# Kernel optimization log

Hardware: AMD Instinct MI355X
Metric: run time of the kernel (lower is better)

The kernel has to match this reference:

```python
import jax, jax.numpy as jnp
import numpy as np
import math

B, T, H, NH, BLOCK = 2, 2048, 1024, 16, 2048
HS = H // NH  # 64, even as required by RoPE


def make_rope_cache(hs, block):
    # positions t = 1..block (note: source starts at 1, not 0)
    t = np.arange(1, block + 1, dtype=np.float32)[:, None]          # (block, 1)
    i = np.arange(1, hs // 2 + 1, dtype=np.float32)[None, :]        # (1, hs/2)
    theta = (1.0 / 10000.0) ** (2.0 * (i - 1.0) / hs)               # (1, hs/2)
    ang = t * theta                                                  # (block, hs/2)
    return jnp.asarray(np.stack([np.cos(ang), np.sin(ang)], axis=-1))  # (block, hs/2, 2)


def setup_inputs() -> dict:
    key = jax.random.key(0)
    ks = jax.random.split(key, 10)
    s = 0.02
    x = jax.random.normal(ks[0], (B, T, H), jnp.float32)
    masks = jax.random.randint(ks[1], (B, T), 0, 2, jnp.int32)  # 1 = padding token
    Wq = jax.random.normal(ks[2], (H, H), jnp.float32) * s
    bq = jnp.zeros((H,), jnp.float32)
    Wk = jax.random.normal(ks[3], (H, H), jnp.float32) * s
    bk = jnp.zeros((H,), jnp.float32)
    Wv = jax.random.normal(ks[4], (H, H), jnp.float32) * s
    bv = jnp.zeros((H,), jnp.float32)
    Wo = jax.random.normal(ks[5], (H, H), jnp.float32) * s  # final_proj, no bias
    rope = make_rope_cache(HS, BLOCK)
    return {"x": x, "masks": masks, "Wq": Wq, "bq": bq, "Wk": Wk, "bk": bk,
            "Wv": Wv, "bv": bv, "Wo": Wo, "rope": rope}


def _apply_rope(x, cos, sin):
    # x: (B, nh, T, hs); cos/sin: (T, hs/2) broadcast over (B, nh)
    xe, xo = x[..., ::2], x[..., 1::2]
    real = cos * xe - sin * xo
    imag = sin * xe + cos * xo
    return jnp.stack([real, imag], axis=-1).reshape(x.shape)


def reference(x, masks, Wq, bq, Wk, bk, Wv, bv, Wo, rope):
    Bn, Tn, Hn = x.shape
    nh, hs = NH, Hn // NH

    def proj(W, b):
        # torch Linear: x @ W.T + b -> (B, nh, T, hs)
        return (x @ W.T + b).reshape(Bn, Tn, nh, hs).transpose(0, 2, 1, 3)

    Q, K, V = proj(Wq, bq), proj(Wk, bk), proj(Wv, bv)
    cos, sin = rope[:Tn, :, 0], rope[:Tn, :, 1]
    Q = _apply_rope(Q, cos, sin)
    K = _apply_rope(K, cos, sin)

    att = jnp.einsum('bhqd,bhkd->bhqk', Q, K) * (1.0 / math.sqrt(hs))
    causal = jnp.tril(jnp.ones((Tn, Tn), bool))
    att = jnp.where(causal[None, None, :, :], att, -1e10)          # causal mask
    att = jnp.where((masks == 1)[:, None, None, :], -1e10, att)   # padding mask on keys
    att = jax.nn.softmax(att, axis=-1)

    y = jnp.einsum('bhqk,bhkd->bhqd', att, V)
    y = y.transpose(0, 2, 1, 3).reshape(Bn, Tn, Hn)
    return y @ Wo.T  # final_proj has no bias
```

## Files before the change

kernel.cpp:

```cpp
#include <hip/hip_runtime.h>

typedef short short8 __attribute__((ext_vector_type(8)));
typedef float floatx4 __attribute__((ext_vector_type(4)));
typedef unsigned short u16;
typedef unsigned long long u64;

#define Tn 2048
#define Kdim 1024
#define QSCALE 0.18033688011112042f
#define FIXEDMAX 20.0f

__device__ inline u16 f2bf(float x) {
    union { float f; unsigned u; } c; c.f = x;
    unsigned u = c.u;
    u += 0x7fffu + ((u >> 16) & 1u);
    return (u16)(u >> 16);
}
__device__ inline float bf2f(u16 h) {
    union { unsigned u; float f; } c; c.u = ((unsigned)h) << 16;
    return c.f;
}
__device__ inline floatx4 mfma16(short8 a, short8 b, floatx4 c) {
    return __builtin_amdgcn_mfma_f32_16x16x32_bf16(a, b, c, 0, 0, 0);
}
__device__ inline void async16(const void* g, void* l) {
    __builtin_amdgcn_global_load_lds((const __attribute__((address_space(1))) void*)g,
                                     (__attribute__((address_space(3))) void*)l, 16, 0, 0);
}

__global__ __launch_bounds__(256) void cvt_all_k(
    const float* __restrict__ x, const float* __restrict__ wq, const float* __restrict__ wk,
    const float* __restrict__ wv, const float* __restrict__ wo, u16* __restrict__ dst)
{
    int i = blockIdx.x * 256 + threadIdx.x;
    const float* s; int off;
    if (i < 1048576) { s = x; off = i; }
    else {
        int j = i - 1048576; int seg = j >> 18; off = j & 262143;
        s = (seg == 0) ? wq : (seg == 1) ? wk : (seg == 2) ? wv : wo;
    }
    float4 v = ((const float4*)s)[off];
    u64 pk = (u64)f2bf(v.x) | ((u64)f2bf(v.y) << 16) | ((u64)f2bf(v.z) << 32) | ((u64)f2bf(v.w) << 48);
    ((u64*)dst)[i] = pk;
}

__global__ __launch_bounds__(256, 5) void gemm_qkv_k(
    const u16* __restrict__ A,
    const u16* __restrict__ W0, const u16* __restrict__ W1, const u16* __restrict__ W2,
    const float* __restrict__ b0, const float* __restrict__ b1, const float* __restrict__ b2,
    u16* o0, u16* o1, u16* o2,
    const float2* __restrict__ rope)
{
    int z = blockIdx.z;
    const u16* W = (z == 0) ? W0 : (z == 1 ? W1 : W2);
    const float* bias = (z == 0) ? b0 : (z == 1 ? b1 : b2);
    u16* outp = (z == 0) ? o0 : (z == 1 ? o1 : o2);

    __shared__ __align__(16) char lds[24576];
    int tid = threadIdx.x;
    int w = tid >> 6, lane = tid & 63, quad = lane >> 4, l15 = lane & 15;
    int m0 = blockIdx.y * 128, n0 = blockIdx.x * 64;
    int wm = w * 32;

    floatx4 acc[2][4];
    floatx4 vzero = {0.f, 0.f, 0.f, 0.f};
#pragma unroll
    for (int i = 0; i < 2; ++i)
#pragma unroll
        for (int j = 0; j < 4; ++j) acc[i][j] = vzero;

    for (int k0 = 0; k0 < Kdim; k0 += 64) {
#pragma unroll
        for (int j = 0; j < 4; ++j) {
            int f = j * 256 + tid, r = f >> 3, c = (f & 7) ^ (r & 7);
            async16(A + (size_t)(m0 + r) * Kdim + k0 + c * 8, lds + j * 4096 + w * 1024);
        }
#pragma unroll
        for (int j = 0; j < 2; ++j) {
            int f = j * 256 + tid, r = f >> 3, c = (f & 7) ^ (r & 7);
            async16(W + (size_t)(n0 + r) * Kdim + k0 + c * 8, lds + 16384 + j * 4096 + w * 1024);
        }
        __syncthreads();
        short8 af[2][2];
#pragma unroll
        for (int mt = 0; mt < 2; ++mt) {
            int ra = wm + mt * 16 + l15;
            const char* pa = lds + ra * 128;
#pragma unroll
            for (int ks = 0; ks < 2; ++ks)
                af[mt][ks] = *(const short8*)(pa + (((ks * 4 + quad) ^ (ra & 7)) << 4));
        }
#pragma unroll
        for (int ks = 0; ks < 2; ++ks)
#pragma unroll
            for (int nt = 0; nt < 4; ++nt) {
                int rb = nt * 16 + l15;
                short8 bf = *(const short8*)(lds + 16384 + rb * 128 + (((ks * 4 + quad) ^ (rb & 7)) << 4));
                acc[0][nt] = mfma16(af[0][ks], bf, acc[0][nt]);
                acc[1][nt] = mfma16(af[1][ks], bf, acc[1][nt]);
            }
        __syncthreads();
    }

    int mbase = m0 + wm;
    if (z <= 1) {
        float osc = (z == 0) ? QSCALE : 1.0f;
#pragma unroll
        for (int nt = 0; nt < 4; ++nt) {
            int col = n0 + nt * 16 + l15;
            float bv = bias[col];
            int p = (col & 63) >> 1;
#pragma unroll
            for (int mt = 0; mt < 2; ++mt) {
                floatx4 a = acc[mt][nt];
#pragma unroll
                for (int r = 0; r < 4; ++r) {
                    int row = mbase + mt * 16 + quad * 4 + r;
                    float v = a[r] + bv;
                    float ov = __shfl_xor(v, 1, 64);
                    float2 cs = rope[(row & (Tn - 1)) * 32 + p];
                    float res = (cs.x * v + ((lane & 1) ? cs.y * ov : -cs.y * ov)) * osc;
                    float pres = __shfl_xor(res, 1, 64);
                    if (!(lane & 1)) {
                        unsigned pk = (unsigned)f2bf(res) | ((unsigned)f2bf(pres) << 16);
                        *(unsigned*)(outp + (size_t)row * 1024 + col) = pk;
                    }
                }
            }
        }
    } else {
#pragma unroll
        for (int nt = 0; nt < 4; ++nt) {
            int col = n0 + nt * 16 + l15;
            float bv = bias[col];
#pragma unroll
            for (int mt = 0; mt < 2; ++mt) {
                floatx4 a = acc[mt][nt];
                int row0 = mbase + mt * 16 + quad * 4;
                int bb = row0 >> 11, t0 = row0 & (Tn - 1);
                u64 pk = (u64)f2bf(a[0] + bv) | ((u64)f2bf(a[1] + bv) << 16)
                       | ((u64)f2bf(a[2] + bv) << 32) | ((u64)f2bf(a[3] + bv) << 48);
                *(u64*)(outp + (size_t)(bb * 1024 + col) * Tn + t0) = pk;
            }
        }
    }
}

__global__ __launch_bounds__(256, 4) void gemm_o_k(
    const u16* __restrict__ A, const u16* __restrict__ W, float* __restrict__ out)
{
    __shared__ __align__(16) char lds[16384];
    int tid = threadIdx.x;
    int w = tid >> 6, lane = tid & 63, quad = lane >> 4, l15 = lane & 15;
    int m0 = blockIdx.y * 64, n0 = blockIdx.x * 64;
    int wm = (w >> 1) * 32, wn = (w & 1) * 32;

    floatx4 acc[2][2];
    floatx4 vzero = {0.f, 0.f, 0.f, 0.f};
#pragma unroll
    for (int i = 0; i < 2; ++i)
#pragma unroll
        for (int j = 0; j < 2; ++j) acc[i][j] = vzero;

    for (int k0 = 0; k0 < Kdim; k0 += 64) {
#pragma unroll
        for (int j = 0; j < 2; ++j) {
            int f = j * 256 + tid, r = f >> 3, c = (f & 7) ^ (r & 7);
            async16(A + (size_t)(m0 + r) * Kdim + k0 + c * 8, lds + j * 4096 + w * 1024);
            async16(W + (size_t)(n0 + r) * Kdim + k0 + c * 8, lds + 8192 + j * 4096 + w * 1024);
        }
        __syncthreads();
        short8 af[2][2];
#pragma unroll
        for (int mt = 0; mt < 2; ++mt) {
            int ra = wm + mt * 16 + l15;
            const char* pa = lds + ra * 128;
#pragma unroll
            for (int ks = 0; ks < 2; ++ks)
                af[mt][ks] = *(const short8*)(pa + (((ks * 4 + quad) ^ (ra & 7)) << 4));
        }
#pragma unroll
        for (int ks = 0; ks < 2; ++ks)
#pragma unroll
            for (int nt = 0; nt < 2; ++nt) {
                int rb = wn + nt * 16 + l15;
                short8 bf = *(const short8*)(lds + 8192 + rb * 128 + (((ks * 4 + quad) ^ (rb & 7)) << 4));
                acc[0][nt] = mfma16(af[0][ks], bf, acc[0][nt]);
                acc[1][nt] = mfma16(af[1][ks], bf, acc[1][nt]);
            }
        __syncthreads();
    }

#pragma unroll
    for (int nt = 0; nt < 2; ++nt) {
        int col = n0 + wn + nt * 16 + l15;
#pragma unroll
        for (int mt = 0; mt < 2; ++mt) {
            floatx4 a = acc[mt][nt];
#pragma unroll
            for (int r = 0; r < 4; ++r) {
                int row = m0 + wm + mt * 16 + quad * 4 + r;
                out[(size_t)row * 1024 + col] = a[r];
            }
        }
    }
}

__global__ __launch_bounds__(64) void vmean_k(const u16* __restrict__ Vt, float* __restrict__ vmean) {
    int row = blockIdx.x;
    int lane = threadIdx.x;
    const u16* p = Vt + (size_t)row * Tn;
    float s = 0.f;
    for (int i = lane * 8; i < Tn; i += 512) {
        short8 v = *(const short8*)(p + i);
#pragma unroll
        for (int j = 0; j < 8; ++j) s += bf2f((u16)v[j]);
    }
#pragma unroll
    for (int off = 1; off < 64; off <<= 1) s += __shfl_xor(s, off, 64);
    if (lane == 0) vmean[row] = s * (1.f / 2048.f);
}

__global__ __launch_bounds__(256) void flash_k(
    const u16* __restrict__ Qb, const u16* __restrict__ Kb, const u16* __restrict__ Vt,
    const int* __restrict__ masks, const float* __restrict__ vmean, u16* __restrict__ Yb)
{
    int bid = blockIdx.x;
    int bh = (bid & 7) * 4 + ((bid >> 3) & 3);
    int qt = 31 - (bid >> 5);
    int b = bh >> 4, h = bh & 15;
    int tid = threadIdx.x, w = tid >> 6, lane = tid & 63, quad = lane >> 4, l15 = lane & 15;
    int sc = (lane & 7) ^ (lane >> 3);

    __shared__ __align__(16) u16 ldsK[2][64 * 64];
    __shared__ __align__(16) u16 ldsV[2][64 * 64];
    __shared__ __align__(16) u16 ldsP[4][16 * 64];

    int ktiles = qt + 1;
    unsigned blo = 0, bhi = 0;
    for (int j = 0; j < ktiles; ++j) {
        u64 mk = __ballot(masks[b * Tn + j * 64 + lane] != 0);
        if (lane == j) { blo = (unsigned)mk; bhi = (unsigned)(mk >> 32); }
    }

    auto stage = [&](int bb, int k0) {
#pragma unroll
        for (int j = 0; j < 2; ++j) {
            int row = j * 32 + w * 8 + (lane >> 3);
            const u16* gk = Kb + (size_t)(b * Tn + k0 + row) * 1024 + h * 64 + sc * 8;
            async16(gk, (char*)&ldsK[bb][0] + (j * 32 + w * 8) * 128);
            const u16* gv = Vt + (size_t)(b * 1024 + h * 64 + row) * Tn + k0 + sc * 8;
            async16(gv, (char*)&ldsV[bb][0] + (j * 32 + w * 8) * 128);
        }
    };
    floatx4 vzero = {0.f, 0.f, 0.f, 0.f};

    int q0 = qt * 64 + w * 16;
    short8 qf[2];
    {
        const u16* qp = Qb + (size_t)(b * Tn + q0 + l15) * 1024 + h * 64 + quad * 8;
        qf[0] = *(const short8*)qp;
        qf[1] = *(const short8*)(qp + 32);
    }
    floatx4 o[4];
    float lsum[4] = {0.f, 0.f, 0.f, 0.f};
#pragma unroll
    for (int i = 0; i < 4; ++i) o[i] = vzero;

    stage(0, 0);
    for (int kt = 0; kt < ktiles; ++kt) {
        int k0 = kt * 64;
        int bb = kt & 1;
        __syncthreads();

        short8 kf[4][2], vf[4][2];
#pragma unroll
        for (int f = 0; f < 4; ++f) {
            int key = f * 16 + l15;
            const char* kbase = (const char*)&ldsK[bb][0] + key * 128;
            const char* vbase = (const char*)&ldsV[bb][0] + key * 128;
#pragma unroll
            for (int ks = 0; ks < 2; ++ks) {
                int slot = ((quad + ks * 4) ^ (key & 7)) << 4;
                kf[f][ks] = *(const short8*)(kbase + slot);
                vf[f][ks] = *(const short8*)(vbase + slot);
            }
        }
        if (kt + 1 < ktiles) stage(bb ^ 1, k0 + 64);

        floatx4 s[4];
#pragma unroll
        for (int f = 0; f < 4; ++f) {
            s[f] = mfma16(qf[0], kf[f][0], vzero);
            s[f] = mfma16(qf[1], kf[f][1], s[f]);
        }

        unsigned mlo = __shfl(blo, kt, 64), mhi = __shfl(bhi, kt, 64);
        int mb[4];
        mb[0] = (mlo >> l15) & 1; mb[1] = (mlo >> (l15 + 16)) & 1;
        mb[2] = (mhi >> l15) & 1; mb[3] = (mhi >> (l15 + 16)) & 1;

        if (k0 + 63 <= q0) {
#pragma unroll
            for (int r = 0; r < 4; ++r) {
                float psum = 0.f;
#pragma unroll
                for (int f = 0; f < 4; ++f) {
                    float v = mb[f] ? -1e10f : s[f][r];
                    float p = __builtin_amdgcn_exp2f(v - FIXEDMAX);
                    psum += p;
                    unsigned u = __float_as_uint(p) + 0x8000u;
                    int row = quad * 4 + r, key = f * 16 + l15;
                    ldsP[w][0] = ldsP[w][0];
                    *((u16*)((char*)&ldsP[w][0] + row * 128 +
                             ((((key >> 3) ^ (row & 7))) << 4) + (key & 7) * 2)) = (u16)(u >> 16);
                }
                lsum[r] += psum;
            }
        } else {
#pragma unroll
            for (int r = 0; r < 4; ++r) {
                int lim = q0 + quad * 4 + r - k0;
                float psum = 0.f;
#pragma unroll
                for (int f = 0; f < 4; ++f) {
                    float v = (16 * f + l15 > lim || mb[f]) ? -1e10f : s[f][r];
                    float p = __builtin_amdgcn_exp2f(v - FIXEDMAX);
                    psum += p;
                    unsigned u = __float_as_uint(p) + 0x8000u;
                    int row = quad * 4 + r, key = f * 16 + l15;
                    *((u16*)((char*)&ldsP[w][0] + row * 128 +
                             ((((key >> 3) ^ (row & 7))) << 4) + (key & 7) * 2)) = (u16)(u >> 16);
                }
                lsum[r] += psum;
            }
        }
        __asm__ volatile("s_waitcnt lgkmcnt(0)" ::: "memory");
        short8 pf0 = *(const short8*)((const char*)&ldsP[w][0] + l15 * 128 + ((quad ^ (l15 & 7)) << 4));
        short8 pf1 = *(const short8*)((const char*)&ldsP[w][0] + l15 * 128 + (((quad + 4) ^ (l15 & 7)) << 4));
#pragma unroll
        for (int nb = 0; nb < 4; ++nb) {
            o[nb] = mfma16(pf0, vf[nb][0], o[nb]);
            o[nb] = mfma16(pf1, vf[nb][1], o[nb]);
        }
    }

#pragma unroll
    for (int r = 0; r < 4; ++r) {
        int qq = q0 + quad * 4 + r;
        float l = lsum[r];
#pragma unroll
        for (int off = 1; off < 16; off <<= 1) l += __shfl_xor(l, off, 64);
        bool degen = (l == 0.f);
        float linv = 1.0f / l;
#pragma unroll
        for (int nb = 0; nb < 4; ++nb) {
            int d = nb * 16 + l15;
            float val = degen ? vmean[b * 1024 + h * 64 + d] : o[nb][r] * linv;
            float pv = __shfl_xor(val, 1, 64);
            if (!(lane & 1)) {
                unsigned pk = (unsigned)f2bf(val) | ((unsigned)f2bf(pv) << 16);
                *(unsigned*)(Yb + (size_t)(b * Tn + qq) * 1024 + h * 64 + d) = pk;
            }
        }
    }
}

extern "C" void kernel_launch(void* const* d_in, const int* in_sizes, int n_in,
                              void* d_out, int out_size, void* d_ws, size_t ws_size,
                              hipStream_t stream) {
    const float* x  = (const float*)d_in[0];
    const int* masks = (const int*)d_in[1];
    const float* Wq = (const float*)d_in[2];
    const float* bq = (const float*)d_in[3];
    const float* Wk = (const float*)d_in[4];
    const float* bk = (const float*)d_in[5];
    const float* Wv = (const float*)d_in[6];
    const float* bv = (const float*)d_in[7];
    const float* Wo = (const float*)d_in[8];
    const float2* rope = (const float2*)d_in[9];
    float* out = (float*)d_out;

    char* ws = (char*)d_ws;
    u16* xb   = (u16*)(ws);
    u16* Wqb  = (u16*)(ws + (8  << 20));
    u16* Wkb  = (u16*)(ws + (10 << 20));
    u16* Wvb  = (u16*)(ws + (12 << 20));
    u16* Wob  = (u16*)(ws + (14 << 20));
    u16* Qb   = (u16*)(ws + (16 << 20));
    u16* Kb2  = (u16*)(ws + (24 << 20));
    u16* Vt   = (u16*)(ws + (32 << 20));
    u16* Yb   = (u16*)(ws + (40 << 20));
    float* vm = (float*)(ws + (48 << 20));

    cvt_all_k<<<8192, 256, 0, stream>>>(x, Wq, Wk, Wv, Wo, xb);

    gemm_qkv_k<<<dim3(16, 32, 3), 256, 0, stream>>>(xb, Wqb, Wkb, Wvb, bq, bk, bv,
                                                    Qb, Kb2, Vt, rope);
    vmean_k<<<2048, 64, 0, stream>>>(Vt, vm);
    flash_k<<<1024, 256, 0, stream>>>(Qb, Kb2, Vt, masks, vm, Yb);
    gemm_o_k<<<dim3(16, 64), 256, 0, stream>>>(Yb, Wob, out);
}
```

Measured before the change: 195.5 us.

## Enlarge GEMM tiles and fold masks into transposed MFMA scores in flash kernel

The QKV projection GEMM now uses 128x128 tiles and the output projection 128x64 tiles, which raises operand reuse per LDS load and cuts the number of blocks. The flash kernel computes the transposed score tile, with K as the A operand, so each lane holds four consecutive keys for one query. The causal and padding masks plus the fixed-max offset are preloaded into the MFMA accumulator, and probabilities are packed with v_cvt_pk_bf16_f32 into 64-bit LDS stores. Row sums are reduced with fewer shuffles. The larger tiles add register and LDS pressure and lower occupancy, and the QKV grid shrinks to 768 blocks.

```diff
diff --git a/kernel.cpp b/kernel.cpp
--- a/kernel.cpp
+++ b/kernel.cpp
@@ -44,7 +44,7 @@
     ((u64*)dst)[i] = pk;
 }
 
-__global__ __launch_bounds__(256, 5) void gemm_qkv_k(
+__global__ __launch_bounds__(256, 3) void gemm_qkv_k(
     const u16* __restrict__ A,
     const u16* __restrict__ W0, const u16* __restrict__ W1, const u16* __restrict__ W2,
     const float* __restrict__ b0, const float* __restrict__ b1, const float* __restrict__ b2,
@@ -56,28 +56,24 @@
     const float* bias = (z == 0) ? b0 : (z == 1 ? b1 : b2);
     u16* outp = (z == 0) ? o0 : (z == 1 ? o1 : o2);
 
-    __shared__ __align__(16) char lds[24576];
+    __shared__ __align__(16) char lds[32768];
     int tid = threadIdx.x;
     int w = tid >> 6, lane = tid & 63, quad = lane >> 4, l15 = lane & 15;
-    int m0 = blockIdx.y * 128, n0 = blockIdx.x * 64;
+    int m0 = blockIdx.y * 128, n0 = blockIdx.x * 128;
     int wm = w * 32;
 
-    floatx4 acc[2][4];
+    floatx4 acc[2][8];
     floatx4 vzero = {0.f, 0.f, 0.f, 0.f};
 #pragma unroll
     for (int i = 0; i < 2; ++i)
 #pragma unroll
-        for (int j = 0; j < 4; ++j) acc[i][j] = vzero;
+        for (int j = 0; j < 8; ++j) acc[i][j] = vzero;
 
     for (int k0 = 0; k0 < Kdim; k0 += 64) {
 #pragma unroll
         for (int j = 0; j < 4; ++j) {
             int f = j * 256 + tid, r = f >> 3, c = (f & 7) ^ (r & 7);
             async16(A + (size_t)(m0 + r) * Kdim + k0 + c * 8, lds + j * 4096 + w * 1024);
-        }
-#pragma unroll
-        for (int j = 0; j < 2; ++j) {
-            int f = j * 256 + tid, r = f >> 3, c = (f & 7) ^ (r & 7);
             async16(W + (size_t)(n0 + r) * Kdim + k0 + c * 8, lds + 16384 + j * 4096 + w * 1024);
         }
         __syncthreads();
@@ -93,7 +89,7 @@
 #pragma unroll
         for (int ks = 0; ks < 2; ++ks)
 #pragma unroll
-            for (int nt = 0; nt < 4; ++nt) {
+            for (int nt = 0; nt < 8; ++nt) {
                 int rb = nt * 16 + l15;
                 short8 bf = *(const short8*)(lds + 16384 + rb * 128 + (((ks * 4 + quad) ^ (rb & 7)) << 4));
                 acc[0][nt] = mfma16(af[0][ks], bf, acc[0][nt]);
@@ -106,7 +102,7 @@
     if (z <= 1) {
         float osc = (z == 0) ? QSCALE : 1.0f;
 #pragma unroll
-        for (int nt = 0; nt < 4; ++nt) {
+        for (int nt = 0; nt < 8; ++nt) {
             int col = n0 + nt * 16 + l15;
             float bv = bias[col];
             int p = (col & 63) >> 1;
@@ -130,7 +126,7 @@
         }
     } else {
 #pragma unroll
-        for (int nt = 0; nt < 4; ++nt) {
+        for (int nt = 0; nt < 8; ++nt) {
             int col = n0 + nt * 16 + l15;
             float bv = bias[col];
 #pragma unroll
@@ -146,28 +142,32 @@
     }
 }
 
-__global__ __launch_bounds__(256, 4) void gemm_o_k(
+__global__ __launch_bounds__(256, 5) void gemm_o_k(
     const u16* __restrict__ A, const u16* __restrict__ W, float* __restrict__ out)
 {
-    __shared__ __align__(16) char lds[16384];
+    __shared__ __align__(16) char lds[24576];
     int tid = threadIdx.x;
     int w = tid >> 6, lane = tid & 63, quad = lane >> 4, l15 = lane & 15;
-    int m0 = blockIdx.y * 64, n0 = blockIdx.x * 64;
-    int wm = (w >> 1) * 32, wn = (w & 1) * 32;
-
-    floatx4 acc[2][2];
+    int m0 = blockIdx.y * 128, n0 = blockIdx.x * 64;
+    int wm = w * 32;
+
+    floatx4 acc[2][4];
     floatx4 vzero = {0.f, 0.f, 0.f, 0.f};
 #pragma unroll
     for (int i = 0; i < 2; ++i)
 #pragma unroll
-        for (int j = 0; j < 2; ++j) acc[i][j] = vzero;
+        for (int j = 0; j < 4; ++j) acc[i][j] = vzero;
 
     for (int k0 = 0; k0 < Kdim; k0 += 64) {
+#pragma unroll
+        for (int j = 0; j < 4; ++j) {
+            int f = j * 256 + tid, r = f >> 3, c = (f & 7) ^ (r & 7);
+            async16(A + (size_t)(m0 + r) * Kdim + k0 + c * 8, lds + j * 4096 + w * 1024);
+        }
 #pragma unroll
         for (int j = 0; j < 2; ++j) {
             int f = j * 256 + tid, r = f >> 3, c = (f & 7) ^ (r & 7);
-            async16(A + (size_t)(m0 + r) * Kdim + k0 + c * 8, lds + j * 4096 + w * 1024);
-            async16(W + (size_t)(n0 + r) * Kdim + k0 + c * 8, lds + 8192 + j * 4096 + w * 1024);
+            async16(W + (size_t)(n0 + r) * Kdim + k0 + c * 8, lds + 16384 + j * 4096 + w * 1024);
         }
         __syncthreads();
         short8 af[2][2];
@@ -182,9 +182,9 @@
 #pragma unroll
         for (int ks = 0; ks < 2; ++ks)
 #pragma unroll
-            for (int nt = 0; nt < 2; ++nt) {
-                int rb = wn + nt * 16 + l15;
-                short8 bf = *(const short8*)(lds + 8192 + rb * 128 + (((ks * 4 + quad) ^ (rb & 7)) << 4));
+            for (int nt = 0; nt < 4; ++nt) {
+                int rb = nt * 16 + l15;
+                short8 bf = *(const short8*)(lds + 16384 + rb * 128 + (((ks * 4 + quad) ^ (rb & 7)) << 4));
                 acc[0][nt] = mfma16(af[0][ks], bf, acc[0][nt]);
                 acc[1][nt] = mfma16(af[1][ks], bf, acc[1][nt]);
             }
@@ -192,8 +192,8 @@
     }
 
 #pragma unroll
-    for (int nt = 0; nt < 2; ++nt) {
-        int col = n0 + wn + nt * 16 + l15;
+    for (int nt = 0; nt < 4; ++nt) {
+        int col = n0 + nt * 16 + l15;
 #pragma unroll
         for (int mt = 0; mt < 2; ++mt) {
             floatx4 a = acc[mt][nt];
@@ -263,9 +263,12 @@
         qf[1] = *(const short8*)(qp + 32);
     }
     floatx4 o[4];
-    float lsum[4] = {0.f, 0.f, 0.f, 0.f};
+    float lsum = 0.f;
 #pragma unroll
     for (int i = 0; i < 4; ++i) o[i] = vzero;
+
+    int sh0 = quad * 4;
+    char* pb = (char*)&ldsP[w][0] + l15 * 128 + ((quad & 1) << 3);
 
     stage(0, 0);
     for (int kt = 0; kt < ktiles; ++kt) {
@@ -288,52 +291,47 @@
         }
         if (kt + 1 < ktiles) stage(bb ^ 1, k0 + 64);
 
+        unsigned mlo = __shfl(blo, kt, 64), mhi = __shfl(bhi, kt, 64);
+        floatx4 ci[4];
+        if (k0 + 63 <= q0) {
+#pragma unroll
+            for (int f = 0; f < 4; ++f) {
+                unsigned nf = (((f & 2) ? mhi : mlo) >> (((f & 1) << 4) + sh0)) & 0xFu;
+#pragma unroll
+                for (int r = 0; r < 4; ++r)
+                    ci[f][r] = ((nf >> r) & 1u) ? -1e10f : -FIXEDMAX;
+            }
+        } else {
+            int dqb = q0 + l15 - k0 - sh0;
+#pragma unroll
+            for (int f = 0; f < 4; ++f) {
+                unsigned nf = (((f & 2) ? mhi : mlo) >> (((f & 1) << 4) + sh0)) & 0xFu;
+                int dq = dqb - f * 16;
+#pragma unroll
+                for (int r = 0; r < 4; ++r)
+                    ci[f][r] = (((nf >> r) & 1u) || (r > dq)) ? -1e10f : -FIXEDMAX;
+            }
+        }
+
         floatx4 s[4];
 #pragma unroll
         for (int f = 0; f < 4; ++f) {
-            s[f] = mfma16(qf[0], kf[f][0], vzero);
-            s[f] = mfma16(qf[1], kf[f][1], s[f]);
-        }
-
-        unsigned mlo = __shfl(blo, kt, 64), mhi = __shfl(bhi, kt, 64);
-        int mb[4];
-        mb[0] = (mlo >> l15) & 1; mb[1] = (mlo >> (l15 + 16)) & 1;
-        mb[2] = (mhi >> l15) & 1; mb[3] = (mhi >> (l15 + 16)) & 1;
-
-        if (k0 + 63 <= q0) {
-#pragma unroll
-            for (int r = 0; r < 4; ++r) {
-                float psum = 0.f;
-#pragma unroll
-                for (int f = 0; f < 4; ++f) {
-                    float v = mb[f] ? -1e10f : s[f][r];
-                    float p = __builtin_amdgcn_exp2f(v - FIXEDMAX);
-                    psum += p;
-                    unsigned u = __float_as_uint(p) + 0x8000u;
-                    int row = quad * 4 + r, key = f * 16 + l15;
-                    ldsP[w][0] = ldsP[w][0];
-                    *((u16*)((char*)&ldsP[w][0] + row * 128 +
-                             ((((key >> 3) ^ (row & 7))) << 4) + (key & 7) * 2)) = (u16)(u >> 16);
-                }
-                lsum[r] += psum;
-            }
-        } else {
-#pragma unroll
-            for (int r = 0; r < 4; ++r) {
-                int lim = q0 + quad * 4 + r - k0;
-                float psum = 0.f;
-#pragma unroll
-                for (int f = 0; f < 4; ++f) {
-                    float v = (16 * f + l15 > lim || mb[f]) ? -1e10f : s[f][r];
-                    float p = __builtin_amdgcn_exp2f(v - FIXEDMAX);
-                    psum += p;
-                    unsigned u = __float_as_uint(p) + 0x8000u;
-                    int row = quad * 4 + r, key = f * 16 + l15;
-                    *((u16*)((char*)&ldsP[w][0] + row * 128 +
-                             ((((key >> 3) ^ (row & 7))) << 4) + (key & 7) * 2)) = (u16)(u >> 16);
-                }
-                lsum[r] += psum;
-            }
+            s[f] = mfma16(kf[f][0], qf[0], ci[f]);
+            s[f] = mfma16(kf[f][1], qf[1], s[f]);
+        }
+
+#pragma unroll
+        for (int f = 0; f < 4; ++f) {
+            float p0 = __builtin_amdgcn_exp2f(s[f][0]);
+            float p1 = __builtin_amdgcn_exp2f(s[f][1]);
+            float p2 = __builtin_amdgcn_exp2f(s[f][2]);
+            float p3 = __builtin_amdgcn_exp2f(s[f][3]);
+            lsum += (p0 + p1) + (p2 + p3);
+            unsigned pka, pkb;
+            asm("v_cvt_pk_bf16_f32 %0, %1, %2" : "=v"(pka) : "v"(p0), "v"(p1));
+            asm("v_cvt_pk_bf16_f32 %0, %1, %2" : "=v"(pkb) : "v"(p2), "v"(p3));
+            u64 pk = (u64)pka | ((u64)pkb << 32);
+            *(u64*)(pb + (((f * 2 + (quad >> 1)) ^ (l15 & 7)) << 4)) = pk;
         }
         __asm__ volatile("s_waitcnt lgkmcnt(0)" ::: "memory");
         short8 pf0 = *(const short8*)((const char*)&ldsP[w][0] + l15 * 128 + ((quad ^ (l15 & 7)) << 4));
@@ -345,12 +343,13 @@
         }
     }
 
+    lsum += __shfl_xor(lsum, 16, 64);
+    lsum += __shfl_xor(lsum, 32, 64);
+
 #pragma unroll
     for (int r = 0; r < 4; ++r) {
         int qq = q0 + quad * 4 + r;
-        float l = lsum[r];
-#pragma unroll
-        for (int off = 1; off < 16; off <<= 1) l += __shfl_xor(l, off, 64);
+        float l = __shfl(lsum, quad * 4 + r, 64);
         bool degen = (l == 0.f);
         float linv = 1.0f / l;
 #pragma unroll
@@ -395,9 +394,9 @@
 
     cvt_all_k<<<8192, 256, 0, stream>>>(x, Wq, Wk, Wv, Wo, xb);
 
-    gemm_qkv_k<<<dim3(16, 32, 3), 256, 0, stream>>>(xb, Wqb, Wkb, Wvb, bq, bk, bv,
-                                                    Qb, Kb2, Vt, rope);
+    gemm_qkv_k<<<dim3(8, 32, 3), 256, 0, stream>>>(xb, Wqb, Wkb, Wvb, bq, bk, bv,
+                                                   Qb, Kb2, Vt, rope);
     vmean_k<<<2048, 64, 0, stream>>>(Vt, vm);
     flash_k<<<1024, 256, 0, stream>>>(Qb, Kb2, Vt, masks, vm, Yb);
-    gemm_o_k<<<dim3(16, 64), 256, 0, stream>>>(Yb, Wob, out);
-}
+    gemm_o_k<<<dim3(16, 32), 256, 0, stream>>>(Yb, Wob, out);
+}
```

Result: slower. 199.5 us (+2.0%).
